# Performance work log

Measured on AMD Instinct MI355X. Metric: run time of the kernel, lower is better.

The kernel has to match this reference:

```python
import jax, jax.numpy as jnp
import numpy as np

B, N_F, N_E = 2, 2048, 4096
FDIM, EDIM, HDIM, HEADS = 128, 128, 64, 4
NEG_INF = -1e9


def setup_inputs() -> dict:
    key = jax.random.key(0)
    ks = jax.random.split(key, 8)
    F0 = jax.random.normal(ks[0], (B, N_F, FDIM), dtype=jnp.float32)
    E0 = jax.random.normal(ks[1], (B, N_E, EDIM), dtype=jnp.float32)
    adj_fe = jax.random.randint(ks[2], (N_F, N_E), 0, 2, dtype=jnp.int32)
    adj_ef = jax.random.randint(ks[3], (N_E, N_F), 0, 2, dtype=jnp.int32)
    # per-head kernels stacked on a leading head axis (same math as the python list)
    sf = float(np.sqrt(6.0 / (FDIM + HDIM)))
    se = float(np.sqrt(6.0 / (EDIM + HDIM)))
    sa = float(np.sqrt(6.0 / (HDIM + 1)))
    Wf = jax.random.uniform(ks[4], (HEADS, FDIM, HDIM), jnp.float32, -sf, sf)
    We = jax.random.uniform(ks[5], (HEADS, EDIM, HDIM), jnp.float32, -se, se)
    a_fe = jax.random.uniform(ks[6], (HEADS, HDIM), jnp.float32, -sa, sa)
    a_ef = jax.random.uniform(ks[7], (HEADS, HDIM), jnp.float32, -sa, sa)
    return {"F0": F0, "E0": E0, "adj_fe": adj_fe, "adj_ef": adj_ef,
            "Wf": Wf, "We": We, "a_fe": a_fe, "a_ef": a_ef}


def _attention(h_src, h_dst, A, a):
    # h_src: [B,H,N,D], h_dst: [B,H,M,D], A: [N,M], a: [H,D]
    e_src = jnp.einsum('bhnd,hd->bhn', h_src, a)
    e_dst = jnp.einsum('bhmd,hd->bhm', h_dst, a)
    e = jax.nn.leaky_relu(e_src[..., :, None] + e_dst[..., None, :], negative_slope=0.2)
    e = jnp.where(A[None, None] > 0, e, NEG_INF)
    alpha = jax.nn.softmax(e, axis=-1)
    # dropout on h_dst is identity at inference (Keras default training=False)
    return jnp.einsum('bhnm,bhmd->bhnd', alpha, h_dst)


def reference(F0, E0, adj_fe, adj_ef, Wf, We, a_fe, a_ef):
    F1 = jnp.einsum('bnf,hfd->bhnd', F0, Wf)  # [B,H,N_F,D]
    E1 = jnp.einsum('bme,hed->bhmd', E0, We)  # [B,H,N_E,D]
    hp_fe = _attention(F1, E1, adj_fe, a_fe)  # [B,H,N_F,D]
    hp_ef = _attention(E1, F1, adj_ef, a_ef)  # [B,H,N_E,D]
    # concat heads on feature axis
    out_fe = jnp.transpose(hp_fe, (0, 2, 1, 3)).reshape(B, N_F, HEADS * HDIM)
    out_ef = jnp.transpose(hp_ef, (0, 2, 1, 3)).reshape(B, N_E, HEADS * HDIM)
    out_fe = jax.nn.softmax(out_fe, axis=-1)
    out_ef = jax.nn.relu(out_ef)
    return (out_fe, out_ef)
```

## Files before the change

kernel.cpp:

```cpp
#include <hip/hip_runtime.h>
#include <hip/hip_bf16.h>
#include <stdint.h>

#define B_  2
#define NF_ 2048
#define NE_ 4096
#define FD_ 128
#define HD_ 64
#define H_  4

#define LOG2E 1.44269504f
#define KH2   4.0f

typedef unsigned long long u64;
typedef __attribute__((ext_vector_type(4))) float f32x4;
typedef __attribute__((ext_vector_type(8))) short bf16x8;
typedef __attribute__((ext_vector_type(8))) _Float16 f16x8;
typedef __attribute__((ext_vector_type(2))) _Float16 f16x2;
typedef __attribute__((ext_vector_type(4))) unsigned uint32x4;

__device__ __forceinline__ float wave_sum64(float v) {
  #pragma unroll
  for (int m = 32; m >= 1; m >>= 1) v += __shfl_xor(v, m, 64);
  return v;
}
__device__ __forceinline__ float wave_max64(float v) {
  #pragma unroll
  for (int m = 32; m >= 1; m >>= 1) v = fmaxf(v, __shfl_xor(v, m, 64));
  return v;
}
__device__ __forceinline__ unsigned short bf16rne(float x) {
  unsigned u = __float_as_uint(x);
  return (unsigned short)((u + 0x7FFFu + ((u >> 16) & 1u)) >> 16);
}
__device__ __forceinline__ f16x2 u2h2(unsigned u) {
  union { unsigned u; f16x2 h; } c; c.u = u; return c.h;
}
__device__ __forceinline__ unsigned h22u(f16x2 h) {
  union { unsigned u; f16x2 h; } c; c.h = h; return c.u;
}
__device__ __forceinline__ unsigned short f16b(float x) {
  union { _Float16 h; unsigned short s; } c; c.h = (_Float16)x; return c.s;
}

__global__ __launch_bounds__(256) void pre_kernel(
    const float* __restrict__ Wf, const float* __restrict__ We,
    const float* __restrict__ a_fe, const float* __restrict__ a_ef,
    __hip_bfloat16* __restrict__ Wfrag, float* __restrict__ Wa)
{
  const int lane = threadIdx.x & 63, wid = threadIdx.x >> 6;
  const int dir = blockIdx.x >> 2, h = blockIdx.x & 3;
  const int cl = lane & 15, kq = lane >> 4;
  const float* W = (dir ? We : Wf) + (size_t)h * FD_ * HD_;
  __hip_bfloat16* fb = Wfrag + (size_t)(dir * 4 + h) * 8192;
  #pragma unroll
  for (int db = 0; db < 4; ++db) {
    unsigned short u[8];
    #pragma unroll
    for (int j = 0; j < 8; ++j)
      u[j] = bf16rne(W[(wid * 32 + kq * 8 + j) * HD_ + db * 16 + cl]);
    uint4 pk;
    pk.x = u[0] | ((unsigned)u[1] << 16);
    pk.y = u[2] | ((unsigned)u[3] << 16);
    pk.z = u[4] | ((unsigned)u[5] << 16);
    pk.w = u[6] | ((unsigned)u[7] << 16);
    *(uint4*)(fb + ((size_t)(wid * 4 + db) * 64 + lane) * 8) = pk;
  }
  if (wid == 0) {
    const float* a1 = a_fe + h * HD_;
    const float* a2 = a_ef + h * HD_;
    float* wa = Wa + (size_t)(dir * 4 + h) * 256;
    #pragma unroll
    for (int rep = 0; rep < 2; ++rep) {
      const int f = lane + rep * 64;
      const float* wr = W + (size_t)f * HD_;
      float s1 = 0.f, s2 = 0.f;
      #pragma unroll 8
      for (int d = 0; d < HD_; ++d) {
        s1 = fmaf(wr[d], a1[d], s1);
        s2 = fmaf(wr[d], a2[d], s2);
      }
      wa[f] = s1 * LOG2E;
      wa[128 + f] = s2 * LOG2E;
    }
  }
}

template<int SWAP, int NN>
__device__ __forceinline__ void proj_mfma(
    const float* __restrict__ X0, const __hip_bfloat16* __restrict__ Wfrag,
    const float* __restrict__ Wa, unsigned short* __restrict__ Vp,
    float2* __restrict__ rowO, unsigned short* __restrict__ colEO,
    unsigned short* __restrict__ colGO, int job, float* __restrict__ ldsX)
{
  const int lane = threadIdx.x & 63;
  const int cl = lane & 15, kq = lane >> 4;
  const int nj = NN >> 4;
  const int nt = job & (nj - 1);
  const int bh = job / nj;
  const int n0 = nt * 16;
  const int h = bh & 3, b = bh >> 2;
  const float* x0 = X0 + ((size_t)b * NN + n0 + cl) * FD_ + kq * 8;
  const __hip_bfloat16* fb = Wfrag + (size_t)((SWAP ? 4 : 0) + h) * 8192;
  const float* wa = Wa + (size_t)((SWAP ? 4 : 0) + h) * 256 + kq * 8;

  bf16x8 wf[4][4];
  #pragma unroll
  for (int ks = 0; ks < 4; ++ks)
    #pragma unroll
    for (int db = 0; db < 4; ++db)
      wf[ks][db] = *(const bf16x8*)(fb + ((size_t)(ks * 4 + db) * 64 + lane) * 8);

  bf16x8 xf[4];
  float d1 = 0.f, d2 = 0.f;
  #pragma unroll
  for (int ks = 0; ks < 4; ++ks) {
    const f32x4 xa = *(const f32x4*)(x0 + ks * 32);
    const f32x4 xb = *(const f32x4*)(x0 + ks * 32 + 4);
    const f32x4 w1a = *(const f32x4*)(wa + ks * 32);
    const f32x4 w1b = *(const f32x4*)(wa + ks * 32 + 4);
    const f32x4 w2a = *(const f32x4*)(wa + 128 + ks * 32);
    const f32x4 w2b = *(const f32x4*)(wa + 128 + ks * 32 + 4);
    #pragma unroll
    for (int i = 0; i < 4; ++i) {
      d1 = fmaf(xa[i], w1a[i], fmaf(xb[i], w1b[i], d1));
      d2 = fmaf(xa[i], w2a[i], fmaf(xb[i], w2b[i], d2));
    }
    #pragma unroll
    for (int i = 0; i < 4; ++i) {
      xf[ks][i]     = (short)bf16rne(xa[i]);
      xf[ks][i + 4] = (short)bf16rne(xb[i]);
    }
  }
  d1 += __shfl_xor(d1, 16, 64); d1 += __shfl_xor(d1, 32, 64);
  d2 += __shfl_xor(d2, 16, 64); d2 += __shfl_xor(d2, 32, 64);

  f32x4 acc[4] = {};
  #pragma unroll
  for (int ks = 0; ks < 4; ++ks)
    #pragma unroll
    for (int db = 0; db < 4; ++db)
      acc[db] = __builtin_amdgcn_mfma_f32_16x16x32_bf16(wf[ks][db], xf[ks],
                                                        acc[db], 0, 0, 0);
  #pragma unroll
  for (int db = 0; db < 4; ++db)
    *(f32x4*)(ldsX + cl * 68 + db * 16 + kq * 4) = acc[db];
  const int mt = n0 >> 6;
  #pragma unroll
  for (int c = 0; c < 2; ++c) {
    const int nb = n0 + c * 8;
    const int ks2 = (nb >> 5) & 1, q2 = (nb >> 3) & 3;
    unsigned short u[8];
    #pragma unroll
    for (int j = 0; j < 8; ++j)
      u[j] = f16b(ldsX[(c * 8 + j) * 68 + lane]);
    uint4 pk;
    pk.x = u[0] | ((unsigned)u[1] << 16);
    pk.y = u[2] | ((unsigned)u[3] << 16);
    pk.z = u[4] | ((unsigned)u[5] << 16);
    pk.w = u[6] | ((unsigned)u[7] << 16);
    *(uint4*)(Vp + ((size_t)((mt * 8 + ks2 * 4 + (lane >> 4)) * 64
                             + q2 * 16 + (lane & 15))) * 8) = pk;
  }
  if (kq == 0) {
    const float rd = SWAP ? d2 : d1;
    const float cd = SWAP ? d1 : d2;
    float2 rp;
    rp.x = exp2f(rd - KH2);
    rp.y = exp2f(0.2f * rd - KH2);
    const size_t idxn = (size_t)bh * NN + n0 + cl;
    rowO[idxn] = rp;
    colEO[idxn] = f16b(exp2f(cd - KH2));
    colGO[idxn] = f16b(exp2f(0.2f * cd - KH2));
  }
}

__device__ __forceinline__ void bitpack_body(
    const int* __restrict__ adj_fe, const int* __restrict__ adj_ef,
    u64* __restrict__ btfe, u64* __restrict__ btef, int id)
{
  const int lane = threadIdx.x & 63;
  const int* adj; u64* bt; int N, M, mt, g;
  if (id < 8192) {
    adj = adj_fe; bt = btfe; N = NF_; M = NE_;
    mt = id >> 7; g = id & 127;
  } else {
    const int k = id - 8192;
    adj = adj_ef; bt = btef; N = NE_; M = NF_;
    mt = k >> 8; g = k & 255;
  }
  const int* base = adj + (size_t)(g * 16) * M + mt * 64 + lane;
  int v[16];
  #pragma unroll
  for (int r = 0; r < 16; ++r) v[r] = base[(size_t)r * M];
  u64 mine = 0;
  #pragma unroll
  for (int r = 0; r < 16; ++r) {
    u64 msk = __ballot(v[r] != 0);
    if (lane == r) mine = msk;
  }
  if (lane < 16) bt[(size_t)mt * N + g * 16 + lane] = mine;
}

__global__ __launch_bounds__(256) void prep_kernel(
    const float* __restrict__ F0, const float* __restrict__ E0,
    const int* __restrict__ adj_fe, const int* __restrict__ adj_ef,
    const __hip_bfloat16* __restrict__ Wfrag, const float* __restrict__ Wa,
    unsigned short* __restrict__ Ftl, unsigned short* __restrict__ Etl,
    float2* __restrict__ rowF, unsigned short* __restrict__ colEF,
    unsigned short* __restrict__ colGF, float2* __restrict__ rowE,
    unsigned short* __restrict__ colEE, unsigned short* __restrict__ colGE,
    u64* __restrict__ btfe, u64* __restrict__ btef)
{
  __shared__ __align__(16) float ldsX[4][16 * 68];
  const int blk = blockIdx.x;
  const int wid = threadIdx.x >> 6;
  if (blk < 4096) {
    bitpack_body(adj_fe, adj_ef, btfe, btef, blk * 4 + wid);
  } else {
    const int job = (blk - 4096) * 4 + wid;
    if (job < 1024) {
      const int bh = job >> 7;
      proj_mfma<0, NF_>(F0, Wfrag, Wa, Ftl + (size_t)bh * 32 * 4096,
                        rowF, colEF, colGF, job, ldsX[wid]);
    } else {
      const int j2 = job - 1024;
      const int bh = j2 >> 8;
      proj_mfma<1, NE_>(E0, Wfrag, Wa, Etl + (size_t)bh * 64 * 4096,
                        rowE, colEE, colGE, j2, ldsX[wid]);
    }
  }
}

template<int TQ, int NN>
__device__ __forceinline__ void attn_wave(
    const unsigned short* __restrict__ vpp, const unsigned short* __restrict__ colE,
    const unsigned short* __restrict__ colG, const u64* __restrict__ bt,
    float Ea, float Ga, int n0, int mt0, int cl, int kq,
    f32x4 (&accT)[4], f32x4 &accS)
{
  const int lane = threadIdx.x & 63;
  f16x8 ones;
  #pragma unroll
  for (int i = 0; i < 8; ++i) ones[i] = (_Float16)1.0f;

  const unsigned short* tb = vpp + (size_t)mt0 * 4096 + (size_t)lane * 8;
  const unsigned short* cpE = colE + mt0 * 64 + kq * 8;
  const unsigned short* cpG = colG + mt0 * 64 + kq * 8;
  const u64* bp = bt + (size_t)mt0 * NN + n0 + cl;
  const int shk = kq * 8;
  const f16x2 Ea2 = {(_Float16)Ea, (_Float16)Ea};
  const f16x2 Ga2 = {(_Float16)Ga, (_Float16)Ga};

  #pragma unroll 1
  for (int t = 0; t < TQ; ++t) {
    const f16x8 vf0 = *(const f16x8*)(tb);
    const f16x8 vf1 = *(const f16x8*)(tb + 512);
    const f16x8 vf2 = *(const f16x8*)(tb + 1024);
    const f16x8 vf3 = *(const f16x8*)(tb + 1536);
    const f16x8 vf4 = *(const f16x8*)(tb + 2048);
    const f16x8 vf5 = *(const f16x8*)(tb + 2560);
    const f16x8 vf6 = *(const f16x8*)(tb + 3072);
    const f16x8 vf7 = *(const f16x8*)(tb + 3584);
    const uint32x4 ceA = *(const uint32x4*)(cpE);
    const uint32x4 ceB = *(const uint32x4*)(cpE + 32);
    const uint32x4 cgA = *(const uint32x4*)(cpG);
    const uint32x4 cgB = *(const uint32x4*)(cpG + 32);
    const u64 s0 = (*bp) >> shk;
    tb += 4096; cpE += 64; cpG += 64; bp += NN;

    uint32x4 pfu;
    unsigned mw;

#define PP(EB, GB, P) {                                                   \
      const f16x2 eb = u2h2((EB)[P]);                                     \
      const f16x2 gb = u2h2((GB)[P]);                                     \
      const f16x2 pm = __builtin_elementwise_max(Ea2 * eb, Ga2 * gb);     \
      const int m0 = __builtin_amdgcn_sbfe((int)mw, 2 * (P), 1);          \
      const int m1 = __builtin_amdgcn_sbfe((int)mw, 2 * (P) + 1, 1);      \
      const unsigned msk = ((unsigned)m0 & 0xFFFFu) |                     \
                           ((unsigned)m1 & 0xFFFF0000u);                  \
      pfu[P] = h22u(pm) & msk;                                            \
    }

    mw = (unsigned)s0;
    PP(ceA, cgA, 0) PP(ceA, cgA, 1) PP(ceA, cgA, 2) PP(ceA, cgA, 3)
    {
      union { uint32x4 u; f16x8 h; } pc; pc.u = pfu;
      const f16x8 pf = pc.h;
      accS = __builtin_amdgcn_mfma_f32_16x16x32_f16(pf, ones, accS, 0, 0, 0);
      accT[0] = __builtin_amdgcn_mfma_f32_16x16x32_f16(pf, vf0, accT[0], 0, 0, 0);
      accT[1] = __builtin_amdgcn_mfma_f32_16x16x32_f16(pf, vf1, accT[1], 0, 0, 0);
      accT[2] = __builtin_amdgcn_mfma_f32_16x16x32_f16(pf, vf2, accT[2], 0, 0, 0);
      accT[3] = __builtin_amdgcn_mfma_f32_16x16x32_f16(pf, vf3, accT[3], 0, 0, 0);
    }
    mw = (unsigned)(s0 >> 32);
    PP(ceB, cgB, 0) PP(ceB, cgB, 1) PP(ceB, cgB, 2) PP(ceB, cgB, 3)
    {
      union { uint32x4 u; f16x8 h; } pc; pc.u = pfu;
      const f16x8 pf = pc.h;
      accS = __builtin_amdgcn_mfma_f32_16x16x32_f16(pf, ones, accS, 0, 0, 0);
      accT[0] = __builtin_amdgcn_mfma_f32_16x16x32_f16(pf, vf4, accT[0], 0, 0, 0);
      accT[1] = __builtin_amdgcn_mfma_f32_16x16x32_f16(pf, vf5, accT[1], 0, 0, 0);
      accT[2] = __builtin_amdgcn_mfma_f32_16x16x32_f16(pf, vf6, accT[2], 0, 0, 0);
      accT[3] = __builtin_amdgcn_mfma_f32_16x16x32_f16(pf, vf7, accT[3], 0, 0, 0);
    }
#undef PP
  }
}

__global__ __launch_bounds__(256) void attn_kernel(
    const unsigned short* __restrict__ Ftl, const unsigned short* __restrict__ Etl,
    const float2* __restrict__ rowF, const unsigned short* __restrict__ colEF,
    const unsigned short* __restrict__ colGF, const float2* __restrict__ rowE,
    const unsigned short* __restrict__ colEE, const unsigned short* __restrict__ colGE,
    const u64* __restrict__ btfe, const u64* __restrict__ btef,
    float* __restrict__ out)
{
  __shared__ __align__(16) float ldsO[4 * 4 * 64 * 4];
  __shared__ float ldsS[4 * 16];

  const int lane = threadIdx.x & 63;
  const int wid  = threadIdx.x >> 6;
  const int cl = lane & 15, kq = lane >> 4;
  const int blk = blockIdx.x;

  int N, bh, n0;
  float* obase;
  bool relu;
  f32x4 accT[4] = {};
  f32x4 accS = {0.f, 0.f, 0.f, 0.f};

  if (blk < 1024) {
    bh = blk & 7;
    n0 = (blk >> 3) * 16;
    N = NF_;
    const float2 rp = rowF[(size_t)bh * NF_ + n0 + cl];
    attn_wave<16, NF_>(Etl + (size_t)bh * 64 * 4096,
                       colEE + (size_t)bh * NE_, colGE + (size_t)bh * NE_,
                       btfe, rp.x, rp.y, n0, wid * 16, cl, kq, accT, accS);
    obase = out; relu = false;
  } else {
    const int k2 = blk - 1024;
    bh = k2 & 7;
    n0 = (k2 >> 3) * 16;
    N = NE_;
    const float2 rp = rowE[(size_t)bh * NE_ + n0 + cl];
    attn_wave<8, NE_>(Ftl + (size_t)bh * 32 * 4096,
                      colEF + (size_t)bh * NF_, colGF + (size_t)bh * NF_,
                      btef, rp.x, rp.y, n0, wid * 8, cl, kq, accT, accS);
    obase = out + (size_t)B_ * NF_ * 256; relu = true;
  }

  #pragma unroll
  for (int db = 0; db < 4; ++db)
    *(f32x4*)&ldsO[((db * 4 + wid) * 64 + lane) * 4] = accT[db];
  if (cl == 0) {
    #pragma unroll
    for (int reg = 0; reg < 4; ++reg)
      ldsS[wid * 16 + kq * 4 + reg] = accS[reg];
  }
  __syncthreads();

  f32x4 osum = {0.f, 0.f, 0.f, 0.f};
  #pragma unroll
  for (int s = 0; s < 4; ++s)
    osum += *(const f32x4*)&ldsO[((wid * 4 + s) * 64 + lane) * 4];
  float stot[4];
  #pragma unroll
  for (int reg = 0; reg < 4; ++reg) {
    stot[reg] = 0.f;
    #pragma unroll
    for (int s = 0; s < 4; ++s) stot[reg] += ldsS[s * 16 + kq * 4 + reg];
  }
  const int b = bh >> 2, h = bh & 3;
  float* orow = obase + ((size_t)b * N + n0 + kq * 4) * 256 + h * HD_ + wid * 16 + cl;
  #pragma unroll
  for (int reg = 0; reg < 4; ++reg) {
    float v = osum[reg] / stot[reg];
    if (relu) v = fmaxf(v, 0.0f);
    orow[reg * 256] = v;
  }
}

__global__ __launch_bounds__(256) void softmax256_kernel(float* __restrict__ io)
{
  const int t = threadIdx.x;
  const int lane = t & 63, wid = t >> 6;
  float v = io[(long)blockIdx.x * 256 + t];
  __shared__ float red[8];
  float m = wave_max64(v);
  if (lane == 0) red[wid] = m;
  __syncthreads();
  m = fmaxf(fmaxf(red[0], red[1]), fmaxf(red[2], red[3]));
  float e = __expf(v - m);
  float s = wave_sum64(e);
  if (lane == 0) red[4 + wid] = s;
  __syncthreads();
  s = (red[4] + red[5]) + (red[6] + red[7]);
  io[(long)blockIdx.x * 256 + t] = e / s;
}

extern "C" void kernel_launch(void* const* d_in, const int* in_sizes, int n_in,
                              void* d_out, int out_size, void* d_ws, size_t ws_size,
                              hipStream_t stream)
{
  const float* F0   = (const float*)d_in[0];
  const float* E0   = (const float*)d_in[1];
  const int* adj_fe = (const int*)d_in[2];
  const int* adj_ef = (const int*)d_in[3];
  const float* Wf   = (const float*)d_in[4];
  const float* We   = (const float*)d_in[5];
  const float* a_fe = (const float*)d_in[6];
  const float* a_ef = (const float*)d_in[7];
  float* out = (float*)d_out;

  char* ws = (char*)d_ws;
  float2* rowF = (float2*)ws;
  float2* rowE = (float2*)(ws + (128 << 10));
  unsigned short* colEF = (unsigned short*)(ws + (384 << 10));
  unsigned short* colGF = (unsigned short*)(ws + (416 << 10));
  unsigned short* colEE = (unsigned short*)(ws + (448 << 10));
  unsigned short* colGE = (unsigned short*)(ws + (512 << 10));
  u64* btfe = (u64*)(ws + (576 << 10));
  u64* btef = btfe + (size_t)NF_ * (NE_ / 64);
  unsigned short* Ftl = (unsigned short*)(btef + (size_t)NE_ * (NF_ / 64));
  unsigned short* Etl = Ftl + (size_t)8 * 32 * 4096;
  __hip_bfloat16* Wfrag = (__hip_bfloat16*)(Etl + (size_t)8 * 64 * 4096);
  float* Wa = (float*)(Wfrag + (size_t)8 * 8192);

  pre_kernel<<<8, 256, 0, stream>>>(Wf, We, a_fe, a_ef, Wfrag, Wa);
  prep_kernel<<<4864, 256, 0, stream>>>(F0, E0, adj_fe, adj_ef, Wfrag, Wa,
                                        Ftl, Etl, rowF, colEF, colGF,
                                        rowE, colEE, colGE, btfe, btef);
  attn_kernel<<<3072, 256, 0, stream>>>(Ftl, Etl, rowF, colEF, colGF,
                                        rowE, colEE, colGE, btfe, btef, out);
  softmax256_kernel<<<B_ * NF_, 256, 0, stream>>>(out);
}
```

Baseline: 88.71 us.

## Process two 16-row query tiles per wave to reuse V fragment loads

Each attention wave now handles 32 query rows (two 16-row tiles) instead of 16. The V tiles and column-score loads are shared across both tiles, which halves global/L2 traffic for V per output row and halves the block count. In exchange, register pressure roughly doubles for accumulators, so waves_per_eu is pinned to 3, and the epilogue runs twice with an extra barrier.

```diff
diff --git a/kernel.cpp b/kernel.cpp
--- a/kernel.cpp
+++ b/kernel.cpp
@@ -233,11 +233,12 @@
 }
 
 template<int TQ, int NN>
-__device__ __forceinline__ void attn_wave(
+__device__ __forceinline__ void attn_wave2(
     const unsigned short* __restrict__ vpp, const unsigned short* __restrict__ colE,
     const unsigned short* __restrict__ colG, const u64* __restrict__ bt,
-    float Ea, float Ga, int n0, int mt0, int cl, int kq,
-    f32x4 (&accT)[4], f32x4 &accS)
+    float Ea0, float Ga0, float Ea1, float Ga1,
+    int n0, int mt0, int cl, int kq,
+    f32x4 (&accT0)[4], f32x4 &accS0, f32x4 (&accT1)[4], f32x4 &accS1)
 {
   const int lane = threadIdx.x & 63;
   f16x8 ones;
@@ -247,10 +248,13 @@
   const unsigned short* tb = vpp + (size_t)mt0 * 4096 + (size_t)lane * 8;
   const unsigned short* cpE = colE + mt0 * 64 + kq * 8;
   const unsigned short* cpG = colG + mt0 * 64 + kq * 8;
-  const u64* bp = bt + (size_t)mt0 * NN + n0 + cl;
+  const u64* bp0 = bt + (size_t)mt0 * NN + n0 + cl;
+  const u64* bp1 = bp0 + 16;
   const int shk = kq * 8;
-  const f16x2 Ea2 = {(_Float16)Ea, (_Float16)Ea};
-  const f16x2 Ga2 = {(_Float16)Ga, (_Float16)Ga};
+  const f16x2 Ea20 = {(_Float16)Ea0, (_Float16)Ea0};
+  const f16x2 Ga20 = {(_Float16)Ga0, (_Float16)Ga0};
+  const f16x2 Ea21 = {(_Float16)Ea1, (_Float16)Ea1};
+  const f16x2 Ga21 = {(_Float16)Ga1, (_Float16)Ga1};
 
   #pragma unroll 1
   for (int t = 0; t < TQ; ++t) {
@@ -266,50 +270,67 @@
     const uint32x4 ceB = *(const uint32x4*)(cpE + 32);
     const uint32x4 cgA = *(const uint32x4*)(cpG);
     const uint32x4 cgB = *(const uint32x4*)(cpG + 32);
-    const u64 s0 = (*bp) >> shk;
-    tb += 4096; cpE += 64; cpG += 64; bp += NN;
-
-    uint32x4 pfu;
-    unsigned mw;
-
-#define PP(EB, GB, P) {                                                   \
+    const u64 s0 = (*bp0) >> shk;
+    const u64 s1 = (*bp1) >> shk;
+    tb += 4096; cpE += 64; cpG += 64; bp0 += NN; bp1 += NN;
+
+    uint32x4 pfu0, pfu1;
+    unsigned mw0, mw1;
+
+#define PP2(EB, GB, P) {                                                  \
       const f16x2 eb = u2h2((EB)[P]);                                     \
       const f16x2 gb = u2h2((GB)[P]);                                     \
-      const f16x2 pm = __builtin_elementwise_max(Ea2 * eb, Ga2 * gb);     \
-      const int m0 = __builtin_amdgcn_sbfe((int)mw, 2 * (P), 1);          \
-      const int m1 = __builtin_amdgcn_sbfe((int)mw, 2 * (P) + 1, 1);      \
-      const unsigned msk = ((unsigned)m0 & 0xFFFFu) |                     \
-                           ((unsigned)m1 & 0xFFFF0000u);                  \
-      pfu[P] = h22u(pm) & msk;                                            \
-    }
-
-    mw = (unsigned)s0;
-    PP(ceA, cgA, 0) PP(ceA, cgA, 1) PP(ceA, cgA, 2) PP(ceA, cgA, 3)
+      const f16x2 pm0 = __builtin_elementwise_max(Ea20 * eb, Ga20 * gb);  \
+      const f16x2 pm1 = __builtin_elementwise_max(Ea21 * eb, Ga21 * gb);  \
+      const int a0 = __builtin_amdgcn_sbfe((int)mw0, 2 * (P), 1);         \
+      const int a1 = __builtin_amdgcn_sbfe((int)mw0, 2 * (P) + 1, 1);     \
+      const int b0 = __builtin_amdgcn_sbfe((int)mw1, 2 * (P), 1);         \
+      const int b1 = __builtin_amdgcn_sbfe((int)mw1, 2 * (P) + 1, 1);     \
+      pfu0[P] = h22u(pm0) & (((unsigned)a0 & 0xFFFFu) |                   \
+                             ((unsigned)a1 & 0xFFFF0000u));               \
+      pfu1[P] = h22u(pm1) & (((unsigned)b0 & 0xFFFFu) |                   \
+                             ((unsigned)b1 & 0xFFFF0000u));               \
+    }
+
+    mw0 = (unsigned)s0; mw1 = (unsigned)s1;
+    PP2(ceA, cgA, 0) PP2(ceA, cgA, 1) PP2(ceA, cgA, 2) PP2(ceA, cgA, 3)
     {
-      union { uint32x4 u; f16x8 h; } pc; pc.u = pfu;
-      const f16x8 pf = pc.h;
-      accS = __builtin_amdgcn_mfma_f32_16x16x32_f16(pf, ones, accS, 0, 0, 0);
-      accT[0] = __builtin_amdgcn_mfma_f32_16x16x32_f16(pf, vf0, accT[0], 0, 0, 0);
-      accT[1] = __builtin_amdgcn_mfma_f32_16x16x32_f16(pf, vf1, accT[1], 0, 0, 0);
-      accT[2] = __builtin_amdgcn_mfma_f32_16x16x32_f16(pf, vf2, accT[2], 0, 0, 0);
-      accT[3] = __builtin_amdgcn_mfma_f32_16x16x32_f16(pf, vf3, accT[3], 0, 0, 0);
-    }
-    mw = (unsigned)(s0 >> 32);
-    PP(ceB, cgB, 0) PP(ceB, cgB, 1) PP(ceB, cgB, 2) PP(ceB, cgB, 3)
+      union { uint32x4 u; f16x8 h; } c0, c1; c0.u = pfu0; c1.u = pfu1;
+      const f16x8 pf0 = c0.h, pf1 = c1.h;
+      accS0 = __builtin_amdgcn_mfma_f32_16x16x32_f16(pf0, ones, accS0, 0, 0, 0);
+      accS1 = __builtin_amdgcn_mfma_f32_16x16x32_f16(pf1, ones, accS1, 0, 0, 0);
+      accT0[0] = __builtin_amdgcn_mfma_f32_16x16x32_f16(pf0, vf0, accT0[0], 0, 0, 0);
+      accT1[0] = __builtin_amdgcn_mfma_f32_16x16x32_f16(pf1, vf0, accT1[0], 0, 0, 0);
+      accT0[1] = __builtin_amdgcn_mfma_f32_16x16x32_f16(pf0, vf1, accT0[1], 0, 0, 0);
+      accT1[1] = __builtin_amdgcn_mfma_f32_16x16x32_f16(pf1, vf1, accT1[1], 0, 0, 0);
+      accT0[2] = __builtin_amdgcn_mfma_f32_16x16x32_f16(pf0, vf2, accT0[2], 0, 0, 0);
+      accT1[2] = __builtin_amdgcn_mfma_f32_16x16x32_f16(pf1, vf2, accT1[2], 0, 0, 0);
+      accT0[3] = __builtin_amdgcn_mfma_f32_16x16x32_f16(pf0, vf3, accT0[3], 0, 0, 0);
+      accT1[3] = __builtin_amdgcn_mfma_f32_16x16x32_f16(pf1, vf3, accT1[3], 0, 0, 0);
+    }
+    mw0 = (unsigned)(s0 >> 32); mw1 = (unsigned)(s1 >> 32);
+    PP2(ceB, cgB, 0) PP2(ceB, cgB, 1) PP2(ceB, cgB, 2) PP2(ceB, cgB, 3)
     {
-      union { uint32x4 u; f16x8 h; } pc; pc.u = pfu;
-      const f16x8 pf = pc.h;
-      accS = __builtin_amdgcn_mfma_f32_16x16x32_f16(pf, ones, accS, 0, 0, 0);
-      accT[0] = __builtin_amdgcn_mfma_f32_16x16x32_f16(pf, vf4, accT[0], 0, 0, 0);
-      accT[1] = __builtin_amdgcn_mfma_f32_16x16x32_f16(pf, vf5, accT[1], 0, 0, 0);
-      accT[2] = __builtin_amdgcn_mfma_f32_16x16x32_f16(pf, vf6, accT[2], 0, 0, 0);
-      accT[3] = __builtin_amdgcn_mfma_f32_16x16x32_f16(pf, vf7, accT[3], 0, 0, 0);
-    }
-#undef PP
-  }
-}
-
-__global__ __launch_bounds__(256) void attn_kernel(
+      union { uint32x4 u; f16x8 h; } c0, c1; c0.u = pfu0; c1.u = pfu1;
+      const f16x8 pf0 = c0.h, pf1 = c1.h;
+      accS0 = __builtin_amdgcn_mfma_f32_16x16x32_f16(pf0, ones, accS0, 0, 0, 0);
+      accS1 = __builtin_amdgcn_mfma_f32_16x16x32_f16(pf1, ones, accS1, 0, 0, 0);
+      accT0[0] = __builtin_amdgcn_mfma_f32_16x16x32_f16(pf0, vf4, accT0[0], 0, 0, 0);
+      accT1[0] = __builtin_amdgcn_mfma_f32_16x16x32_f16(pf1, vf4, accT1[0], 0, 0, 0);
+      accT0[1] = __builtin_amdgcn_mfma_f32_16x16x32_f16(pf0, vf5, accT0[1], 0, 0, 0);
+      accT1[1] = __builtin_amdgcn_mfma_f32_16x16x32_f16(pf1, vf5, accT1[1], 0, 0, 0);
+      accT0[2] = __builtin_amdgcn_mfma_f32_16x16x32_f16(pf0, vf6, accT0[2], 0, 0, 0);
+      accT1[2] = __builtin_amdgcn_mfma_f32_16x16x32_f16(pf1, vf6, accT1[2], 0, 0, 0);
+      accT0[3] = __builtin_amdgcn_mfma_f32_16x16x32_f16(pf0, vf7, accT0[3], 0, 0, 0);
+      accT1[3] = __builtin_amdgcn_mfma_f32_16x16x32_f16(pf1, vf7, accT1[3], 0, 0, 0);
+    }
+#undef PP2
+  }
+}
+
+__global__ __launch_bounds__(256)
+__attribute__((amdgpu_waves_per_eu(3, 3)))
+void attn_kernel(
     const unsigned short* __restrict__ Ftl, const unsigned short* __restrict__ Etl,
     const float2* __restrict__ rowF, const unsigned short* __restrict__ colEF,
     const unsigned short* __restrict__ colGF, const float2* __restrict__ rowE,
@@ -328,58 +349,93 @@
   int N, bh, n0;
   float* obase;
   bool relu;
-  f32x4 accT[4] = {};
-  f32x4 accS = {0.f, 0.f, 0.f, 0.f};
-
-  if (blk < 1024) {
+  f32x4 accT0[4] = {}, accT1[4] = {};
+  f32x4 accS0 = {0.f, 0.f, 0.f, 0.f}, accS1 = {0.f, 0.f, 0.f, 0.f};
+
+  if (blk < 512) {
     bh = blk & 7;
-    n0 = (blk >> 3) * 16;
+    n0 = (blk >> 3) * 32;
     N = NF_;
-    const float2 rp = rowF[(size_t)bh * NF_ + n0 + cl];
-    attn_wave<16, NF_>(Etl + (size_t)bh * 64 * 4096,
-                       colEE + (size_t)bh * NE_, colGE + (size_t)bh * NE_,
-                       btfe, rp.x, rp.y, n0, wid * 16, cl, kq, accT, accS);
+    const float2 r0 = rowF[(size_t)bh * NF_ + n0 + cl];
+    const float2 r1 = rowF[(size_t)bh * NF_ + n0 + 16 + cl];
+    attn_wave2<16, NF_>(Etl + (size_t)bh * 64 * 4096,
+                        colEE + (size_t)bh * NE_, colGE + (size_t)bh * NE_,
+                        btfe, r0.x, r0.y, r1.x, r1.y,
+                        n0, wid * 16, cl, kq, accT0, accS0, accT1, accS1);
     obase = out; relu = false;
   } else {
-    const int k2 = blk - 1024;
+    const int k2 = blk - 512;
     bh = k2 & 7;
-    n0 = (k2 >> 3) * 16;
+    n0 = (k2 >> 3) * 32;
     N = NE_;
-    const float2 rp = rowE[(size_t)bh * NE_ + n0 + cl];
-    attn_wave<8, NE_>(Ftl + (size_t)bh * 32 * 4096,
-                      colEF + (size_t)bh * NF_, colGF + (size_t)bh * NF_,
-                      btef, rp.x, rp.y, n0, wid * 8, cl, kq, accT, accS);
+    const float2 r0 = rowE[(size_t)bh * NE_ + n0 + cl];
+    const float2 r1 = rowE[(size_t)bh * NE_ + n0 + 16 + cl];
+    attn_wave2<8, NE_>(Ftl + (size_t)bh * 32 * 4096,
+                       colEF + (size_t)bh * NF_, colGF + (size_t)bh * NF_,
+                       btef, r0.x, r0.y, r1.x, r1.y,
+                       n0, wid * 8, cl, kq, accT0, accS0, accT1, accS1);
     obase = out + (size_t)B_ * NF_ * 256; relu = true;
   }
 
+  const int b = bh >> 2, h = bh & 3;
   #pragma unroll
   for (int db = 0; db < 4; ++db)
-    *(f32x4*)&ldsO[((db * 4 + wid) * 64 + lane) * 4] = accT[db];
+    *(f32x4*)&ldsO[((db * 4 + wid) * 64 + lane) * 4] = accT0[db];
   if (cl == 0) {
     #pragma unroll
     for (int reg = 0; reg < 4; ++reg)
-      ldsS[wid * 16 + kq * 4 + reg] = accS[reg];
+      ldsS[wid * 16 + kq * 4 + reg] = accS0[reg];
   }
   __syncthreads();
-
-  f32x4 osum = {0.f, 0.f, 0.f, 0.f};
-  #pragma unroll
-  for (int s = 0; s < 4; ++s)
-    osum += *(const f32x4*)&ldsO[((wid * 4 + s) * 64 + lane) * 4];
-  float stot[4];
-  #pragma unroll
-  for (int reg = 0; reg < 4; ++reg) {
-    stot[reg] = 0.f;
-    #pragma unroll
-    for (int s = 0; s < 4; ++s) stot[reg] += ldsS[s * 16 + kq * 4 + reg];
-  }
-  const int b = bh >> 2, h = bh & 3;
-  float* orow = obase + ((size_t)b * N + n0 + kq * 4) * 256 + h * HD_ + wid * 16 + cl;
-  #pragma unroll
-  for (int reg = 0; reg < 4; ++reg) {
-    float v = osum[reg] / stot[reg];
-    if (relu) v = fmaxf(v, 0.0f);
-    orow[reg * 256] = v;
+  {
+    f32x4 osum = {0.f, 0.f, 0.f, 0.f};
+    #pragma unroll
+    for (int s = 0; s < 4; ++s)
+      osum += *(const f32x4*)&ldsO[((wid * 4 + s) * 64 + lane) * 4];
+    float stot[4];
+    #pragma unroll
+    for (int reg = 0; reg < 4; ++reg) {
+      stot[reg] = 0.f;
+      #pragma unroll
+      for (int s = 0; s < 4; ++s) stot[reg] += ldsS[s * 16 + kq * 4 + reg];
+    }
+    float* orow = obase + ((size_t)b * N + n0 + kq * 4) * 256 + h * HD_ + wid * 16 + cl;
+    #pragma unroll
+    for (int reg = 0; reg < 4; ++reg) {
+      float v = osum[reg] / stot[reg];
+      if (relu) v = fmaxf(v, 0.0f);
+      orow[reg * 256] = v;
+    }
+  }
+  __syncthreads();
+  #pragma unroll
+  for (int db = 0; db < 4; ++db)
+    *(f32x4*)&ldsO[((db * 4 + wid) * 64 + lane) * 4] = accT1[db];
+  if (cl == 0) {
+    #pragma unroll
+    for (int reg = 0; reg < 4; ++reg)
+      ldsS[wid * 16 + kq * 4 + reg] = accS1[reg];
+  }
+  __syncthreads();
+  {
+    f32x4 osum = {0.f, 0.f, 0.f, 0.f};
+    #pragma unroll
+    for (int s = 0; s < 4; ++s)
+      osum += *(const f32x4*)&ldsO[((wid * 4 + s) * 64 + lane) * 4];
+    float stot[4];
+    #pragma unroll
+    for (int reg = 0; reg < 4; ++reg) {
+      stot[reg] = 0.f;
+      #pragma unroll
+      for (int s = 0; s < 4; ++s) stot[reg] += ldsS[s * 16 + kq * 4 + reg];
+    }
+    float* orow = obase + ((size_t)b * N + n0 + 16 + kq * 4) * 256 + h * HD_ + wid * 16 + cl;
+    #pragma unroll
+    for (int reg = 0; reg < 4; ++reg) {
+      float v = osum[reg] / stot[reg];
+      if (relu) v = fmaxf(v, 0.0f);
+      orow[reg * 256] = v;
+    }
   }
 }
 
@@ -433,7 +489,7 @@
   prep_kernel<<<4864, 256, 0, stream>>>(F0, E0, adj_fe, adj_ef, Wfrag, Wa,
                                         Ftl, Etl, rowF, colEF, colGF,
                                         rowE, colEE, colGE, btfe, btef);
-  attn_kernel<<<3072, 256, 0, stream>>>(Ftl, Etl, rowF, colEF, colGF,
+  attn_kernel<<<1536, 256, 0, stream>>>(Ftl, Etl, rowF, colEF, colGF,
                                         rowE, colEE, colGE, btfe, btef, out);
   softmax256_kernel<<<B_ * NF_, 256, 0, stream>>>(out);
 }
```

New measurement: 74.54 us, median of 2. -16.0%, faster.
